# Performance work log

Measured on AMD Instinct MI355X. Metric: run time of the kernel, lower is better.

The kernel has to match this reference:

```python
import jax, jax.numpy as jnp
import numpy as np

B, S, H = 8, 512, 1024          # batch, seq_len, hidden_size
T, K, FF = 8, 2, 4096           # num_thoughts, top_k, ffn dim (4*H)
NH = 8                          # combiner attention heads
HD = H // NH
CREATIVITY = 1.0


def setup_inputs() -> dict:
    key = jax.random.key(0)
    ks = jax.random.split(key, 16)
    s = 0.02
    return {
        "hidden_states": jax.random.normal(ks[0], (B, S, H), jnp.float32),
        # router
        "router_w": jax.random.normal(ks[1], (H, T), jnp.float32) * s,
        "router_b": jnp.zeros((T,), jnp.float32),
        # thought branch FFNs (one per thought)
        "W1": jax.random.normal(ks[2], (T, H, FF), jnp.float32) * s,
        "b1": jnp.zeros((T, FF), jnp.float32),
        "W2": jax.random.normal(ks[3], (T, FF, H), jnp.float32) * s,
        "b2": jnp.zeros((T, H), jnp.float32),
        # attention combiner (MultiheadAttention proj weights)
        "Wq": jax.random.normal(ks[4], (H, H), jnp.float32) * s,
        "bq": jnp.zeros((H,), jnp.float32),
        "Wk": jax.random.normal(ks[5], (H, H), jnp.float32) * s,
        "bk": jnp.zeros((H,), jnp.float32),
        "Wv": jax.random.normal(ks[6], (H, H), jnp.float32) * s,
        "bv": jnp.zeros((H,), jnp.float32),
        "Wo": jax.random.normal(ks[7], (H, H), jnp.float32) * s,
        "bo": jnp.zeros((H,), jnp.float32),
    }


def reference(hidden_states, router_w, router_b, W1, b1, W2, b2,
              Wq, bq, Wk, bk, Wv, bv, Wo, bo):
    # ---- router: mean-pool -> linear -> softmax -> top-k ----
    pooled = hidden_states.mean(axis=1)                       # [B,H]
    router_probs = jax.nn.softmax(pooled @ router_w + router_b, axis=-1)  # [B,T]
    top_p, top_i = jax.lax.top_k(router_probs, K)             # [B,K]
    weights = jax.nn.softmax(top_p, axis=-1)                  # renormalized active weights [B,K]

    # ---- grouped branch FFN (gather expert weights, batched GEMMs) ----
    h = jnp.einsum('bsh,bkhf->bksf', hidden_states, W1[top_i]) + b1[top_i][:, :, None, :]
    h = jax.nn.gelu(h, approximate=False)
    branch_out = jnp.einsum('bksf,bkfh->bksh', h, W2[top_i]) + b2[top_i][:, :, None, :]
    branch_out = branch_out * CREATIVITY                      # [B,K,S,H]

    # ---- attention combiner over flattened thoughts [B, K*S, H] ----
    L = K * S
    flat = branch_out.reshape(B, L, H)
    q = (flat @ Wq + bq).reshape(B, L, NH, HD)
    k = (flat @ Wk + bk).reshape(B, L, NH, HD)
    v = (flat @ Wv + bv).reshape(B, L, NH, HD)
    scores = jnp.einsum('blhd,bmhd->bhlm', q, k) / jnp.sqrt(jnp.float32(HD))
    attn = jax.nn.softmax(scores, axis=-1)
    ctx = jnp.einsum('bhlm,bmhd->blhd', attn, v).reshape(B, L, H)
    attended = (ctx @ Wo + bo).reshape(B, K, S, H)

    combined = jnp.einsum('bksh,bk->bsh', attended, weights)  # [B,S,H]

    # ---- metrics ----
    entropy = jnp.mean(-jnp.sum(router_probs * jnp.log(router_probs + 1e-8), axis=1))
    a = branch_out[:, 0].reshape(B, -1)
    b_ = branch_out[:, 1].reshape(B, -1)
    cos = jnp.sum(a * b_, -1) / jnp.maximum(
        jnp.linalg.norm(a, axis=-1) * jnp.linalg.norm(b_, axis=-1), 1e-8)
    diversity = jnp.mean(1.0 - cos)
    return combined, entropy, diversity
```

## Files before the change

kernel.cpp:

```cpp
#include <hip/hip_runtime.h>
#include <hip/hip_bf16.h>
#include <math.h>

typedef float f32x4 __attribute__((ext_vector_type(4)));
typedef short s16x8 __attribute__((ext_vector_type(8)));
typedef short s16x4 __attribute__((ext_vector_type(4)));
typedef unsigned int u32;

#define DEVI __device__ __forceinline__

#define Bn   8
#define Sn   512
#define Hn   1024
#define Tn   8
#define Kn   2
#define FFn  4096
#define NHn  8
#define HDn  128
#define Ln   1024
#define OUT_COMBINED 4194304

DEVI unsigned short f2bf(float x) {
  __hip_bfloat16 h = __float2bfloat16(x);
  union { __hip_bfloat16 h; unsigned short u; } cv; cv.h = h; return cv.u;
}
DEVI float bf2f(unsigned short u) {
  union { u32 i; float f; } cv; cv.i = ((u32)u) << 16; return cv.f;
}
DEVI float gelu_f(float x) {
  float t = x * x * x;
  float y = 0.7978845608028654f * x + 0.03567740813f * t;
  float e = exp2f(2.8853900817779268f * y);
  return x - x / (e + 1.0f);
}

typedef __attribute__((address_space(3))) u32 lds_u32;
typedef __attribute__((address_space(1))) u32 glb_u32;
DEVI void gload16(const void* g, void* l) {
  __builtin_amdgcn_global_load_lds((const glb_u32*)g, (lds_u32*)l, 16, 0, 0);
}

__global__ __launch_bounds__(256) void pool_part_k(const float* __restrict__ hid, float* __restrict__ part)
{
  const int b = blockIdx.x, scn = blockIdx.y;
  const int hh = threadIdx.x * 4;
  float4 acc = make_float4(0.f, 0.f, 0.f, 0.f);
  const float* base = hid + ((long)b * Sn + (long)scn * 128) * Hn + hh;
  for (int s = 0; s < 128; ++s) {
    float4 v = *(const float4*)(base + (long)s * Hn);
    acc.x += v.x; acc.y += v.y; acc.z += v.z; acc.w += v.w;
  }
  *(float4*)(part + ((long)(scn * Bn + b)) * Hn + hh) = acc;
}

__global__ __launch_bounds__(256) void pool_final_k(const float* __restrict__ part, float* __restrict__ pooled)
{
  const int i = blockIdx.x * 256 + threadIdx.x;
  float s = 0.f;
  for (int sc = 0; sc < 4; ++sc) s += part[sc * (Bn * Hn) + i];
  pooled[i] = s * (1.f / (float)Sn);
}

__global__ __launch_bounds__(256) void router_k(
    const float* __restrict__ pooled, const float* __restrict__ rw, const float* __restrict__ rb,
    float* __restrict__ probs, int* __restrict__ topi, float* __restrict__ wts,
    int* __restrict__ flags, float* __restrict__ entropy_out)
{
  __shared__ float partial[256];
  __shared__ float lg[64];
  __shared__ int sfl[8];
  __shared__ float sent[8];
  const int tid = threadIdx.x;
  const int bt = tid & 63, slice = tid >> 6;
  const int b = bt >> 3, t = bt & 7;
  if (tid < 8) sfl[tid] = 0;
  float acc = 0.f;
  const float* pb = pooled + b * Hn;
  for (int i = slice * 256; i < slice * 256 + 256; ++i) acc += pb[i] * rw[i * Tn + t];
  partial[tid] = acc;
  __syncthreads();
  if (tid < 64) lg[tid] = rb[t] + partial[tid] + partial[tid + 64] + partial[tid + 128] + partial[tid + 192];
  __syncthreads();
  if (tid < 64 && t == 0) {
    float p[8];
    float mx = lg[b * 8];
    for (int i = 1; i < 8; ++i) mx = fmaxf(mx, lg[b * 8 + i]);
    float ssum = 0.f;
    for (int i = 0; i < 8; ++i) { p[i] = expf(lg[b * 8 + i] - mx); ssum += p[i]; }
    float ent = 0.f;
    for (int i = 0; i < 8; ++i) { p[i] /= ssum; ent -= p[i] * logf(p[i] + 1e-8f); probs[b * 8 + i] = p[i]; }
    sent[b] = ent;
    int i1 = 0;
    for (int i = 1; i < 8; ++i) if (p[i] > p[i1]) i1 = i;
    int i2 = (i1 == 0) ? 1 : 0;
    for (int i = 0; i < 8; ++i) if (i != i1 && p[i] > p[i2]) i2 = i;
    float w0 = 1.f / (1.f + expf(p[i2] - p[i1]));
    float w1 = 1.f / (1.f + expf(p[i1] - p[i2]));
    topi[b * 2] = i1; topi[b * 2 + 1] = i2;
    wts[b * 2] = w0; wts[b * 2 + 1] = w1;
    atomicOr(&sfl[i1], 1); atomicOr(&sfl[i2], 1);
  }
  __syncthreads();
  if (tid < 8) flags[tid] = sfl[tid];
  if (tid == 0) {
    float e = 0.f;
    for (int i = 0; i < 8; ++i) e += sent[i];
    entropy_out[0] = e * (1.f / (float)Bn);
  }
}

__global__ __launch_bounds__(256) void cvt_k(const float* __restrict__ in, unsigned short* __restrict__ out)
{
  const long i = ((long)blockIdx.x * 256 + threadIdx.x) * 4;
  float4 v = *(const float4*)(in + i);
  s16x4 o;
  o[0] = (short)f2bf(v.x); o[1] = (short)f2bf(v.y); o[2] = (short)f2bf(v.z); o[3] = (short)f2bf(v.w);
  *(s16x4*)(out + i) = o;
}

__global__ __launch_bounds__(256) void bias3_k(const float* __restrict__ bq, const float* __restrict__ bk,
                                               const float* __restrict__ bv, float* __restrict__ o)
{
  const int i = blockIdx.x * 256 + threadIdx.x;
  o[i] = bq[i]; o[i + 1024] = bk[i]; o[i + 2048] = bv[i];
}

__global__ __launch_bounds__(256) void transpose_k(const float* __restrict__ Win, unsigned short* __restrict__ Wout,
                                                   int Kd, int N, long sIn, long sOut, const int* __restrict__ flags)
{
  const int t = blockIdx.z;
  if (flags && flags[t] == 0) return;
  __shared__ float tile[64][65];
  const float* in = Win + (long)t * sIn;
  unsigned short* out = Wout + (long)t * sOut;
  const int kb = blockIdx.y * 64, nb = blockIdx.x * 64;
  const int tx = threadIdx.x & 15, ty = threadIdx.x >> 4;
  #pragma unroll
  for (int i = 0; i < 4; ++i) {
    const int r = ty + i * 16;
    float4 v = *(const float4*)(in + (long)(kb + r) * N + nb + tx * 4);
    tile[r][tx * 4 + 0] = v.x; tile[r][tx * 4 + 1] = v.y;
    tile[r][tx * 4 + 2] = v.z; tile[r][tx * 4 + 3] = v.w;
  }
  __syncthreads();
  #pragma unroll
  for (int i = 0; i < 4; ++i) {
    const int n = ty + i * 16;
    s16x4 o;
    #pragma unroll
    for (int j = 0; j < 4; ++j) o[j] = (short)f2bf(tile[tx * 4 + j][n]);
    *(s16x4*)(out + (long)(nb + n) * Kd + kb + tx * 4) = o;
  }
}

template<int EPI, int OUTMODE>
__global__ __launch_bounds__(256, 2) void gemmT_k(
    const unsigned short* __restrict__ A0, const unsigned short* __restrict__ Bt0,
    const float* __restrict__ bias0, unsigned short* __restrict__ C0,
    int N, int Kd,
    const int* __restrict__ topi, int kTop,
    long sA_b, long sA_p, long sBt_t, int sBias_t, long sC_p)
{
  __shared__ __align__(16) char smem[73728];
  char* const Ab = smem;
  char* const Bb = smem + 49152;

  const int gx = gridDim.x, gy = gridDim.y;
  const int nwg = gx * gy * gridDim.z;
  const int hw = blockIdx.x + gx * (blockIdx.y + gy * blockIdx.z);
  const int q = nwg >> 3, r = nwg & 7;
  const int xcd = hw & 7, sub = hw >> 3;
  int lin = (xcd < r ? xcd * (q + 1) : r * (q + 1) + (xcd - r) * q) + sub;
  const int bx = lin % gx; lin /= gx;
  const int by = lin % gy;
  const int bz = lin / gy;

  const int bidx = kTop ? (bz / kTop) : 0;
  const int te = topi ? topi[bz] : 0;
  const unsigned short* A = A0 + (long)bidx * sA_b + (long)bz * sA_p;
  const unsigned short* Bt = Bt0 + (long)te * sBt_t;
  const float* bias = bias0 + (long)te * sBias_t;
  unsigned short* C = C0 + (long)bz * sC_p;

  const int m0 = by * 256;
  const int n0 = bx * 128;
  const int tid = threadIdx.x;
  const int lane = tid & 63, w = tid >> 6;
  const int wm = w >> 1, wn = w & 1;
  const int rA = lane & 15, g = lane >> 4;

  const int sr = lane >> 2;
  const int sc = lane & 3;
  const int csw = (sc ^ ((sr & 3) ^ ((sr >> 2) & 3))) * 8;
  const unsigned short* gAw = A + (long)(m0 + w * 64 + sr) * Kd + csw;
  const unsigned short* gBw = Bt + (long)(n0 + w * 32 + sr) * Kd + csw;
  const int ldso = lane << 4;

  const int sl = (rA & 3) ^ ((rA >> 2) & 3);
  int aoff[8], boff[4];
  #pragma unroll
  for (int mi = 0; mi < 8; ++mi)
    aoff[mi] = (wm * 128 + mi * 16 + rA) * 64 + ((g ^ sl) << 4);
  #pragma unroll
  for (int nj = 0; nj < 4; ++nj)
    boff[nj] = (wn * 64 + nj * 16 + rA) * 64 + ((g ^ sl) << 4);

  f32x4 acc[8][4];
  const f32x4 zero = {0.f, 0.f, 0.f, 0.f};
  #pragma unroll
  for (int i = 0; i < 8; ++i)
    #pragma unroll
    for (int j = 0; j < 4; ++j) acc[i][j] = zero;

  const int nt = Kd >> 5;

  auto stageA = [&](int kt2, int buf, int i) {
    gload16(gAw + (long)i * 16 * Kd + kt2 * 32, Ab + buf * 16384 + w * 4096 + i * 1024 + ldso);
  };
  auto stageB = [&](int kt2, int buf, int i) {
    gload16(gBw + (long)i * 16 * Kd + kt2 * 32, Bb + buf * 8192 + w * 2048 + i * 1024 + ldso);
  };

  #pragma unroll
  for (int j = 0; j < 2; ++j) {
    stageA(j, j, 0); stageA(j, j, 1); stageB(j, j, 0);
    stageA(j, j, 2); stageA(j, j, 3); stageB(j, j, 1);
  }
  asm volatile("s_waitcnt vmcnt(6)" ::: "memory");
  __builtin_amdgcn_s_barrier();

  int cb = 0, fb = 2;
  for (int kt = 0; kt < nt; ++kt) {
    const char* pa = Ab + cb * 16384;
    const char* pb = Bb + cb * 8192;
    const bool st = (kt + 2 < nt);
    const int ft = kt + 2;

    s16x8 af[8], bf[4];
    #pragma unroll
    for (int mi = 0; mi < 4; ++mi) af[mi] = *(const s16x8*)(pa + aoff[mi]);
    #pragma unroll
    for (int nj = 0; nj < 4; ++nj) bf[nj] = *(const s16x8*)(pb + boff[nj]);
    if (st) { stageA(ft, fb, 0); stageA(ft, fb, 1); stageB(ft, fb, 0); }
    #pragma unroll
    for (int mi = 0; mi < 4; ++mi) af[4 + mi] = *(const s16x8*)(pa + aoff[4 + mi]);
    if (st) { stageA(ft, fb, 2); stageA(ft, fb, 3); stageB(ft, fb, 1); }

    __builtin_amdgcn_s_setprio(1);
    #pragma unroll
    for (int mi = 0; mi < 8; ++mi)
      #pragma unroll
      for (int nj = 0; nj < 4; ++nj)
        acc[mi][nj] = __builtin_amdgcn_mfma_f32_16x16x32_bf16(af[mi], bf[nj], acc[mi][nj], 0, 0, 0);
    __builtin_amdgcn_s_setprio(0);

    if (st)                asm volatile("s_waitcnt vmcnt(6) lgkmcnt(0)" ::: "memory");
    else if (kt + 1 < nt)  asm volatile("s_waitcnt vmcnt(0) lgkmcnt(0)" ::: "memory");
    else                   asm volatile("s_waitcnt lgkmcnt(0)" ::: "memory");
    __builtin_amdgcn_s_barrier();
    cb = (cb + 1 == 3) ? 0 : cb + 1;
    fb = (fb + 1 == 3) ? 0 : fb + 1;
  }

  __syncthreads();

  unsigned short* et = (unsigned short*)(smem + w * 9216);
  const int r4 = (lane >> 4) << 2;
  const int nbase = n0 + wn * 64;
  const int seg = (OUTMODE == 1) ? (nbase >> 10) : 0;
  const int erow = lane >> 3, echunk = lane & 7;
  float bv[4];
  #pragma unroll
  for (int nj = 0; nj < 4; ++nj) bv[nj] = bias[nbase + nj * 16 + rA];

  #pragma unroll
  for (int p = 0; p < 2; ++p) {
    #pragma unroll
    for (int nj = 0; nj < 4; ++nj) {
      #pragma unroll
      for (int mi2 = 0; mi2 < 4; ++mi2) {
        #pragma unroll
        for (int j = 0; j < 4; ++j) {
          float x = acc[p * 4 + mi2][nj][j] + bv[nj];
          if (EPI == 1) x = gelu_f(x);
          const int mrl = mi2 * 16 + r4 + j;
          const int ncl = nj * 16 + rA;
          if (OUTMODE == 0 || seg < 2) et[mrl * 72 + ncl] = f2bf(x);
          else                         et[ncl * 72 + mrl] = f2bf(x);
        }
      }
    }
    const long mrow0 = m0 + wm * 128 + p * 64;
    if (OUTMODE == 0) {
      #pragma unroll
      for (int rr = 0; rr < 8; ++rr) {
        const int row = rr * 8 + erow;
        s16x8 v = *(const s16x8*)(et + row * 72 + echunk * 8);
        *(s16x8*)(C + (mrow0 + row) * N + nbase + echunk * 8) = v;
      }
    } else {
      const int nseg = nbase & 1023;
      if (seg < 2) {
        unsigned short* dst = C + (long)seg * 8388608;
        #pragma unroll
        for (int rr = 0; rr < 8; ++rr) {
          const int row = rr * 8 + erow;
          s16x8 v = *(const s16x8*)(et + row * 72 + echunk * 8);
          *(s16x8*)(dst + (mrow0 + row) * 1024 + nseg + echunk * 8) = v;
        }
      } else {
        unsigned short* vtp = C + 16777216;
        const int bb = (int)(mrow0 >> 10);
        const int ltok0 = (int)(mrow0 & 1023);
        #pragma unroll
        for (int rr = 0; rr < 8; ++rr) {
          const int nrow = rr * 8 + erow;
          s16x8 v = *(const s16x8*)(et + nrow * 72 + echunk * 8);
          *(s16x8*)(vtp + ((long)(bb * 1024 + nseg + nrow)) * 1024 + ltok0 + echunk * 8) = v;
        }
      }
    }
  }
}

__global__ __launch_bounds__(256) void flash_k(
    const unsigned short* __restrict__ q, const unsigned short* __restrict__ k,
    const unsigned short* __restrict__ vt, unsigned short* __restrict__ ctx)
{
  __shared__ unsigned short Ks[64 * 128];
  __shared__ unsigned short Vs[128 * 64];
  __shared__ unsigned short Ps[4][32 * 72];
  const int qt = blockIdx.x, h = blockIdx.y, b = blockIdx.z;
  const int tid = threadIdx.x, lane = tid & 63, w = tid >> 6;
  const int rA = lane & 15, g = lane >> 4;
  const int q0w = qt * 128 + w * 32;

  s16x8 qf[2][4];
  #pragma unroll
  for (int qi = 0; qi < 2; ++qi) {
    const unsigned short* qp = q + ((long)(b * Ln + q0w + qi * 16 + rA)) * Hn + h * HDn + g * 8;
    #pragma unroll
    for (int kk = 0; kk < 4; ++kk) qf[qi][kk] = *(const s16x8*)(qp + kk * 32);
  }

  f32x4 o[2][8];
  const f32x4 zero = {0.f, 0.f, 0.f, 0.f};
  #pragma unroll
  for (int qi = 0; qi < 2; ++qi)
    #pragma unroll
    for (int nn = 0; nn < 8; ++nn) o[qi][nn] = zero;
  float lrun[2][4];
  #pragma unroll
  for (int qi = 0; qi < 2; ++qi)
    #pragma unroll
    for (int j = 0; j < 4; ++j) lrun[qi][j] = 0.f;
  float m = 0.f;

  const float sc2 = 0.08838834764831845f * 1.4426950408889634f;

  const int krow0 = w * 16 + g;
  const int kc = lane & 15;
  const int vrow0 = w * 32 + (lane >> 3);
  const int vc = lane & 7;

  for (int kvt = 0; kvt < 16; ++kvt) {
    const int kv0 = kvt * 64;
    __syncthreads();
    #pragma unroll
    for (int qq = 0; qq < 4; ++qq) {
      const int rk = krow0 + qq * 4;
      gload16(k + ((long)(b * Ln + kv0 + rk)) * Hn + h * HDn + ((kc ^ (rk & 7)) * 8),
              (char*)Ks + w * 4096 + qq * 1024);
      const int rv = vrow0 + qq * 8;
      gload16(vt + ((long)(b * 1024 + h * HDn + rv)) * Ln + kv0 + ((vc ^ (rv & 7)) * 8),
              (char*)Vs + w * 4096 + qq * 1024);
    }
    __syncthreads();

    f32x4 sacc[2][4];
    #pragma unroll
    for (int qi = 0; qi < 2; ++qi)
      #pragma unroll
      for (int nj = 0; nj < 4; ++nj) sacc[qi][nj] = zero;
    #pragma unroll
    for (int kk = 0; kk < 4; ++kk) {
      #pragma unroll
      for (int nj = 0; nj < 4; ++nj) {
        const int row = nj * 16 + rA;
        const int byt = row * 256 + (((kk * 4 + g) ^ (row & 7)) << 4);
        s16x8 kf = *(const s16x8*)((const char*)Ks + byt);
        sacc[0][nj] = __builtin_amdgcn_mfma_f32_16x16x32_bf16(qf[0][kk], kf, sacc[0][nj], 0, 0, 0);
        sacc[1][nj] = __builtin_amdgcn_mfma_f32_16x16x32_bf16(qf[1][kk], kf, sacc[1][nj], 0, 0, 0);
      }
    }

    float vmax = -3.0e38f;
    #pragma unroll
    for (int qi = 0; qi < 2; ++qi)
      #pragma unroll
      for (int nj = 0; nj < 4; ++nj)
        #pragma unroll
        for (int j = 0; j < 4; ++j) {
          const float s = sacc[qi][nj][j] * sc2;
          sacc[qi][nj][j] = s;
          vmax = fmaxf(vmax, s);
        }
    if (!__all(vmax <= m + 8.0f)) {
      float mn = vmax;
      #pragma unroll
      for (int mm = 1; mm < 64; mm <<= 1) mn = fmaxf(mn, __shfl_xor(mn, mm, 64));
      const float al = exp2f(m - mn);
      #pragma unroll
      for (int qi = 0; qi < 2; ++qi) {
        #pragma unroll
        for (int nn = 0; nn < 8; ++nn)
          #pragma unroll
          for (int j = 0; j < 4; ++j) o[qi][nn][j] *= al;
        #pragma unroll
        for (int j = 0; j < 4; ++j) lrun[qi][j] *= al;
      }
      m = mn;
    }
    #pragma unroll
    for (int qi = 0; qi < 2; ++qi)
      #pragma unroll
      for (int j = 0; j < 4; ++j) {
        float p0 = exp2f(sacc[qi][0][j] - m);
        float p1 = exp2f(sacc[qi][1][j] - m);
        float p2 = exp2f(sacc[qi][2][j] - m);
        float p3 = exp2f(sacc[qi][3][j] - m);
        lrun[qi][j] += (p0 + p1) + (p2 + p3);
        const int prow = (qi * 16 + g * 4 + j) * 72;
        Ps[w][prow + 0 * 16 + rA] = f2bf(p0);
        Ps[w][prow + 1 * 16 + rA] = f2bf(p1);
        Ps[w][prow + 2 * 16 + rA] = f2bf(p2);
        Ps[w][prow + 3 * 16 + rA] = f2bf(p3);
      }

    s16x8 pf[2][2];
    #pragma unroll
    for (int qi = 0; qi < 2; ++qi)
      #pragma unroll
      for (int kk2 = 0; kk2 < 2; ++kk2)
        pf[qi][kk2] = *(const s16x8*)(&Ps[w][(qi * 16 + rA) * 72 + kk2 * 32 + g * 8]);
    #pragma unroll
    for (int kk2 = 0; kk2 < 2; ++kk2) {
      #pragma unroll
      for (int nn = 0; nn < 8; ++nn) {
        const int row = nn * 16 + rA;
        const int byt = row * 128 + (((kk2 * 4 + g) ^ (row & 7)) << 4);
        s16x8 vf = *(const s16x8*)((const char*)Vs + byt);
        o[0][nn] = __builtin_amdgcn_mfma_f32_16x16x32_bf16(pf[0][kk2], vf, o[0][nn], 0, 0, 0);
        o[1][nn] = __builtin_amdgcn_mfma_f32_16x16x32_bf16(pf[1][kk2], vf, o[1][nn], 0, 0, 0);
      }
    }
  }

  float linv[2][4];
  #pragma unroll
  for (int qi = 0; qi < 2; ++qi)
    #pragma unroll
    for (int j = 0; j < 4; ++j) {
      float l = lrun[qi][j];
      #pragma unroll
      for (int mm = 1; mm < 16; mm <<= 1) l += __shfl_xor(l, mm, 64);
      linv[qi][j] = 1.0f / l;
    }
  #pragma unroll
  for (int qi = 0; qi < 2; ++qi)
    #pragma unroll
    for (int nn = 0; nn < 8; ++nn)
      #pragma unroll
      for (int j = 0; j < 4; ++j) {
        const int row = q0w + qi * 16 + g * 4 + j;
        ctx[((long)(b * Ln + row)) * Hn + h * HDn + nn * 16 + rA] = f2bf(o[qi][nn][j] * linv[qi][j]);
      }
}

__global__ __launch_bounds__(256) void div_part_k(const unsigned short* __restrict__ br, float* __restrict__ part)
{
  const int b = blockIdx.y, ch = blockIdx.x;
  const unsigned short* a = br + (long)b * (2L * Sn * Hn);
  const unsigned short* c = a + (long)Sn * Hn;
  const int base = ch * 16384 + threadIdx.x * 8;
  float dot = 0.f, na = 0.f, nb = 0.f;
  #pragma unroll
  for (int i = 0; i < 8; ++i) {
    const int idx = base + i * 2048;
    s16x8 av = *(const s16x8*)(a + idx);
    s16x8 cv = *(const s16x8*)(c + idx);
    #pragma unroll
    for (int e = 0; e < 8; ++e) {
      float fa = bf2f((unsigned short)av[e]);
      float fc = bf2f((unsigned short)cv[e]);
      dot += fa * fc; na += fa * fa; nb += fc * fc;
    }
  }
  #pragma unroll
  for (int mm = 1; mm < 64; mm <<= 1) {
    dot += __shfl_xor(dot, mm, 64);
    na  += __shfl_xor(na, mm, 64);
    nb  += __shfl_xor(nb, mm, 64);
  }
  __shared__ float red[12];
  const int lane = threadIdx.x & 63, w = threadIdx.x >> 6;
  if (lane == 0) { red[w * 3] = dot; red[w * 3 + 1] = na; red[w * 3 + 2] = nb; }
  __syncthreads();
  if (threadIdx.x == 0) {
    float d = 0, x = 0, y = 0;
    for (int i = 0; i < 4; ++i) { d += red[i * 3]; x += red[i * 3 + 1]; y += red[i * 3 + 2]; }
    float* op = part + ((long)(b * 32 + ch)) * 3;
    op[0] = d; op[1] = x; op[2] = y;
  }
}

__global__ __launch_bounds__(64) void div_final_k(const float* __restrict__ part, float* __restrict__ outp)
{
  __shared__ float cosr[8];
  const int tid = threadIdx.x;
  if (tid < 8) {
    float d = 0, x = 0, y = 0;
    for (int i = 0; i < 32; ++i) {
      const float* p = part + ((long)(tid * 32 + i)) * 3;
      d += p[0]; x += p[1]; y += p[2];
    }
    cosr[tid] = d / fmaxf(sqrtf(x) * sqrtf(y), 1e-8f);
  }
  __syncthreads();
  if (tid == 0) {
    float s = 0.f;
    for (int i = 0; i < 8; ++i) s += 1.f - cosr[i];
    outp[0] = s * (1.f / 8.f);
  }
}

__global__ __launch_bounds__(256) void combine_k(const unsigned short* __restrict__ att,
                                                 const float* __restrict__ wts, float* __restrict__ out)
{
  const long i = ((long)blockIdx.x * 256 + threadIdx.x) * 8;
  const int b = (int)(i >> 19);
  const long rem = i & 524287;
  const unsigned short* a0 = att + (long)b * (2L * Sn * Hn) + rem;
  const unsigned short* a1 = a0 + (long)Sn * Hn;
  const float w0 = wts[b * 2], w1 = wts[b * 2 + 1];
  s16x8 v0 = *(const s16x8*)a0;
  s16x8 v1 = *(const s16x8*)a1;
  float r[8];
  #pragma unroll
  for (int e = 0; e < 8; ++e) r[e] = w0 * bf2f((unsigned short)v0[e]) + w1 * bf2f((unsigned short)v1[e]);
  *(float4*)(out + i)     = make_float4(r[0], r[1], r[2], r[3]);
  *(float4*)(out + i + 4) = make_float4(r[4], r[5], r[6], r[7]);
}

extern "C" void kernel_launch(void* const* d_in, const int* in_sizes, int n_in,
                              void* d_out, int out_size, void* d_ws, size_t ws_size,
                              hipStream_t stream)
{
  (void)in_sizes; (void)n_in; (void)out_size; (void)ws_size;
  const float* hidden   = (const float*)d_in[0];
  const float* router_w = (const float*)d_in[1];
  const float* router_b = (const float*)d_in[2];
  const float* W1 = (const float*)d_in[3];
  const float* b1 = (const float*)d_in[4];
  const float* W2 = (const float*)d_in[5];
  const float* b2 = (const float*)d_in[6];
  const float* Wq = (const float*)d_in[7];
  const float* bq = (const float*)d_in[8];
  const float* Wk = (const float*)d_in[9];
  const float* bk = (const float*)d_in[10];
  const float* Wv = (const float*)d_in[11];
  const float* bv = (const float*)d_in[12];
  const float* Wo = (const float*)d_in[13];
  const float* bo = (const float*)d_in[14];
  float* out = (float*)d_out;

  char* ws = (char*)d_ws;
  float* pooled  = (float*)(ws);
  float* ppart   = (float*)(ws + 32768);
  float* probs   = (float*)(ws + 163840);
  int*   topi    = (int*)  (ws + 164096);
  float* wts     = (float*)(ws + 164352);
  int*   flags   = (int*)  (ws + 164608);
  float* dpart   = (float*)(ws + 164864);
  float* qkvbias = (float*)(ws + 167936);
  unsigned short* hid_bf = (unsigned short*)(ws + 262144);
  unsigned short* Wt     = (unsigned short*)(ws + 262144 + 8388608);
  unsigned short* hbuf   = (unsigned short*)(ws + 262144 + 8388608 + 67108864);
  unsigned short* br     = (unsigned short*)(ws + 262144 + 8388608 + 134217728);
  unsigned short* wqkvo  = (unsigned short*)(ws + 262144 + 8388608 + 134217728 + 16777216);
  unsigned short* qb  = Wt;
  unsigned short* kbf = Wt + 8388608;
  unsigned short* vt  = Wt + 16777216;
  unsigned short* ctx = hbuf;
  unsigned short* att = hbuf + 8388608;
  unsigned short* wqt = wqkvo;
  unsigned short* wkt = wqkvo + 1048576;
  unsigned short* wvt = wqkvo + 2097152;
  unsigned short* wot = wqkvo + 3145728;

  pool_part_k<<<dim3(Bn, 4), 256, 0, stream>>>(hidden, ppart);
  pool_final_k<<<dim3(32), 256, 0, stream>>>(ppart, pooled);
  router_k<<<1, 256, 0, stream>>>(pooled, router_w, router_b, probs, topi, wts, flags, out + OUT_COMBINED);

  cvt_k<<<4096, 256, 0, stream>>>(hidden, hid_bf);
  bias3_k<<<4, 256, 0, stream>>>(bq, bk, bv, qkvbias);
  transpose_k<<<dim3(64, 16, Tn), 256, 0, stream>>>(W1, Wt, Hn, FFn, (long)Hn * FFn, (long)FFn * Hn, flags);
  transpose_k<<<dim3(16, 16, 1), 256, 0, stream>>>(Wq, wqt, Hn, Hn, 0, 0, nullptr);
  transpose_k<<<dim3(16, 16, 1), 256, 0, stream>>>(Wk, wkt, Hn, Hn, 0, 0, nullptr);
  transpose_k<<<dim3(16, 16, 1), 256, 0, stream>>>(Wv, wvt, Hn, Hn, 0, 0, nullptr);
  transpose_k<<<dim3(16, 16, 1), 256, 0, stream>>>(Wo, wot, Hn, Hn, 0, 0, nullptr);

  gemmT_k<1, 0><<<dim3(FFn / 128, Sn / 256, 16), 256, 0, stream>>>(
      hid_bf, Wt, b1, hbuf, FFn, Hn, topi, 2,
      (long)Sn * Hn, 0L, (long)FFn * Hn, FFn, (long)Sn * FFn);

  transpose_k<<<dim3(16, 64, Tn), 256, 0, stream>>>(W2, Wt, FFn, Hn, (long)FFn * Hn, (long)Hn * FFn, flags);

  gemmT_k<0, 0><<<dim3(Hn / 128, Sn / 256, 16), 256, 0, stream>>>(
      hbuf, Wt, b2, br, Hn, FFn, topi, 2,
      0L, (long)Sn * FFn, (long)Hn * FFn, Hn, (long)Sn * Hn);

  div_part_k<<<dim3(32, Bn), 256, 0, stream>>>(br, dpart);
  div_final_k<<<1, 64, 0, stream>>>(dpart, out + OUT_COMBINED + 1);

  gemmT_k<0, 1><<<dim3(3072 / 128, (Bn * Ln) / 256, 1), 256, 0, stream>>>(
      br, wqkvo, qkvbias, qb, 3072, Hn, nullptr, 0, 0L, 0L, 0L, 0, 0L);

  flash_k<<<dim3(Ln / 128, NHn, Bn), 256, 0, stream>>>(qb, kbf, vt, ctx);

  gemmT_k<0, 0><<<dim3(Hn / 128, (Bn * Ln) / 256, 1), 256, 0, stream>>>(
      ctx, wot, bo, att, Hn, Hn, nullptr, 0, 0L, 0L, 0L, 0, 0L);

  combine_k<<<2048, 256, 0, stream>>>(att, wts, out);
}
```

Baseline: 517.7 us.

## Use 256x256 8-wave GEMM tiles with split-K for FFN2

```diff
diff --git a/kernel.cpp b/kernel.cpp
--- a/kernel.cpp
+++ b/kernel.cpp
@@ -123,6 +123,7 @@
 {
   const int i = blockIdx.x * 256 + threadIdx.x;
   o[i] = bq[i]; o[i + 1024] = bk[i]; o[i + 2048] = bv[i];
+  o[i + 3072] = 0.f;
 }
 
 __global__ __launch_bounds__(256) void transpose_k(const float* __restrict__ Win, unsigned short* __restrict__ Wout,
@@ -153,17 +154,18 @@
   }
 }
 
-template<int EPI, int OUTMODE>
-__global__ __launch_bounds__(256, 2) void gemmT_k(
+template<int EPI, int OUTMODE, int KSPLIT>
+__global__ __launch_bounds__(512, 1) void gemm8_k(
     const unsigned short* __restrict__ A0, const unsigned short* __restrict__ Bt0,
-    const float* __restrict__ bias0, unsigned short* __restrict__ C0,
-    int N, int Kd,
+    const float* __restrict__ bias0, const float* __restrict__ zbias,
+    unsigned short* __restrict__ C0,
+    int N, int Kd, int Klen,
     const int* __restrict__ topi, int kTop,
-    long sA_b, long sA_p, long sBt_t, int sBias_t, long sC_p)
-{
-  __shared__ __align__(16) char smem[73728];
+    long sA_b, long sA_p, long sBt_t, int sBias_t, long sC_p, long sC_k)
+{
+  __shared__ __align__(16) char smem[131072];
   char* const Ab = smem;
-  char* const Bb = smem + 49152;
+  char* const Bb = smem + 65536;
 
   const int gx = gridDim.x, gy = gridDim.y;
   const int nwg = gx * gy * gridDim.z;
@@ -175,35 +177,51 @@
   const int by = lin % gy;
   const int bz = lin / gy;
 
-  const int bidx = kTop ? (bz / kTop) : 0;
-  const int te = topi ? topi[bz] : 0;
-  const unsigned short* A = A0 + (long)bidx * sA_b + (long)bz * sA_p;
-  const unsigned short* Bt = Bt0 + (long)te * sBt_t;
-  const float* bias = bias0 + (long)te * sBias_t;
-  unsigned short* C = C0 + (long)bz * sC_p;
+  const int zp = KSPLIT ? (bz >> 1) : bz;
+  const int ks = KSPLIT ? (bz & 1) : 0;
+  const int bidx = kTop ? (zp / kTop) : 0;
+  const int te = topi ? topi[zp] : 0;
+  const unsigned short* A = A0 + (long)bidx * sA_b + (long)zp * sA_p + ks * 2048;
+  const unsigned short* Bt = Bt0 + (long)te * sBt_t + ks * 2048;
+  const float* bias = (KSPLIT && ks) ? zbias : (bias0 + (long)te * sBias_t);
+  unsigned short* C = C0 + (long)zp * sC_p + (long)ks * sC_k;
 
   const int m0 = by * 256;
-  const int n0 = bx * 128;
+  const int n0 = bx * 256;
   const int tid = threadIdx.x;
   const int lane = tid & 63, w = tid >> 6;
-  const int wm = w >> 1, wn = w & 1;
+  const int wm = w >> 2, wn = w & 3;
   const int rA = lane & 15, g = lane >> 4;
 
-  const int sr = lane >> 2;
-  const int sc = lane & 3;
-  const int csw = (sc ^ ((sr & 3) ^ ((sr >> 2) & 3))) * 8;
-  const unsigned short* gAw = A + (long)(m0 + w * 64 + sr) * Kd + csw;
-  const unsigned short* gBw = Bt + (long)(n0 + w * 32 + sr) * Kd + csw;
-  const int ldso = lane << 4;
-
-  const int sl = (rA & 3) ^ ((rA >> 2) & 3);
+  const int srow = tid >> 2;
+  const int sc = tid & 3;
+  const int csw = (sc ^ ((srow & 3) ^ ((srow >> 2) & 3))) * 8;
+  const unsigned short* gA0p = A + (long)(m0 + srow) * Kd + csw;
+  const unsigned short* gA1p = A + (long)(m0 + srow + 128) * Kd + csw;
+  const unsigned short* gB0p = Bt + (long)(n0 + srow) * Kd + csw;
+  const unsigned short* gB1p = Bt + (long)(n0 + srow + 128) * Kd + csw;
+
+  auto stA = [&](int kt2, int buf, int kh) {
+    const long ko = (long)kt2 * 64 + kh * 32;
+    char* d = Ab + buf * 32768 + kh * 16384 + tid * 16;
+    gload16(gA0p + ko, d);
+    gload16(gA1p + ko, d + 8192);
+  };
+  auto stB = [&](int kt2, int buf, int kh) {
+    const long ko = (long)kt2 * 64 + kh * 32;
+    char* d = Bb + buf * 32768 + kh * 16384 + tid * 16;
+    gload16(gB0p + ko, d);
+    gload16(gB1p + ko, d + 8192);
+  };
+
+  const int chsw = (g ^ ((rA & 3) ^ ((rA >> 2) & 3))) << 4;
   int aoff[8], boff[4];
   #pragma unroll
   for (int mi = 0; mi < 8; ++mi)
-    aoff[mi] = (wm * 128 + mi * 16 + rA) * 64 + ((g ^ sl) << 4);
+    aoff[mi] = (wm * 128 + mi * 16 + rA) * 64 + chsw;
   #pragma unroll
   for (int nj = 0; nj < 4; ++nj)
-    boff[nj] = (wn * 64 + nj * 16 + rA) * 64 + ((g ^ sl) << 4);
+    boff[nj] = (wn * 64 + nj * 16 + rA) * 64 + chsw;
 
   f32x4 acc[8][4];
   const f32x4 zero = {0.f, 0.f, 0.f, 0.f};
@@ -212,60 +230,99 @@
     #pragma unroll
     for (int j = 0; j < 4; ++j) acc[i][j] = zero;
 
-  const int nt = Kd >> 5;
-
-  auto stageA = [&](int kt2, int buf, int i) {
-    gload16(gAw + (long)i * 16 * Kd + kt2 * 32, Ab + buf * 16384 + w * 4096 + i * 1024 + ldso);
-  };
-  auto stageB = [&](int kt2, int buf, int i) {
-    gload16(gBw + (long)i * 16 * Kd + kt2 * 32, Bb + buf * 8192 + w * 2048 + i * 1024 + ldso);
-  };
-
-  #pragma unroll
-  for (int j = 0; j < 2; ++j) {
-    stageA(j, j, 0); stageA(j, j, 1); stageB(j, j, 0);
-    stageA(j, j, 2); stageA(j, j, 3); stageB(j, j, 1);
-  }
-  asm volatile("s_waitcnt vmcnt(6)" ::: "memory");
+  const int nt = Klen >> 6;
+
+  stA(0, 0, 0); stB(0, 0, 0); stA(0, 0, 1); stB(0, 0, 1);
+  asm volatile("s_waitcnt vmcnt(4)" ::: "memory");
   __builtin_amdgcn_s_barrier();
 
-  int cb = 0, fb = 2;
   for (int kt = 0; kt < nt; ++kt) {
-    const char* pa = Ab + cb * 16384;
-    const char* pb = Bb + cb * 8192;
-    const bool st = (kt + 2 < nt);
-    const int ft = kt + 2;
-
-    s16x8 af[8], bf[4];
-    #pragma unroll
-    for (int mi = 0; mi < 4; ++mi) af[mi] = *(const s16x8*)(pa + aoff[mi]);
-    #pragma unroll
-    for (int nj = 0; nj < 4; ++nj) bf[nj] = *(const s16x8*)(pb + boff[nj]);
-    if (st) { stageA(ft, fb, 0); stageA(ft, fb, 1); stageB(ft, fb, 0); }
-    #pragma unroll
-    for (int mi = 0; mi < 4; ++mi) af[4 + mi] = *(const s16x8*)(pa + aoff[4 + mi]);
-    if (st) { stageA(ft, fb, 2); stageA(ft, fb, 3); stageB(ft, fb, 1); }
-
+    const char* paA = Ab + (kt & 1) * 32768;
+    const char* paB = Bb + (kt & 1) * 32768;
+    const int fb = (kt & 1) ^ 1;
+    const bool st = (kt + 1 < nt);
+    s16x8 af[4], bf[4];
+
+    #pragma unroll
+    for (int mi = 0; mi < 4; ++mi) af[mi] = *(const s16x8*)(paA + aoff[mi]);
+    #pragma unroll
+    for (int nj = 0; nj < 4; ++nj) bf[nj] = *(const s16x8*)(paB + boff[nj]);
+    if (st) stA(kt + 1, fb, 0);
+    __builtin_amdgcn_sched_barrier(0);
+    __builtin_amdgcn_s_barrier();
+    asm volatile("s_waitcnt lgkmcnt(0)" ::: "memory");
+    __builtin_amdgcn_sched_barrier(0);
     __builtin_amdgcn_s_setprio(1);
     #pragma unroll
-    for (int mi = 0; mi < 8; ++mi)
+    for (int mi = 0; mi < 4; ++mi)
       #pragma unroll
       for (int nj = 0; nj < 4; ++nj)
         acc[mi][nj] = __builtin_amdgcn_mfma_f32_16x16x32_bf16(af[mi], bf[nj], acc[mi][nj], 0, 0, 0);
     __builtin_amdgcn_s_setprio(0);
-
-    if (st)                asm volatile("s_waitcnt vmcnt(6) lgkmcnt(0)" ::: "memory");
-    else if (kt + 1 < nt)  asm volatile("s_waitcnt vmcnt(0) lgkmcnt(0)" ::: "memory");
-    else                   asm volatile("s_waitcnt lgkmcnt(0)" ::: "memory");
+    __builtin_amdgcn_sched_barrier(0);
     __builtin_amdgcn_s_barrier();
-    cb = (cb + 1 == 3) ? 0 : cb + 1;
-    fb = (fb + 1 == 3) ? 0 : fb + 1;
+
+    #pragma unroll
+    for (int mi = 0; mi < 4; ++mi) af[mi] = *(const s16x8*)(paA + aoff[4 + mi]);
+    if (st) stB(kt + 1, fb, 0);
+    __builtin_amdgcn_sched_barrier(0);
+    __builtin_amdgcn_s_barrier();
+    asm volatile("s_waitcnt lgkmcnt(0)" ::: "memory");
+    __builtin_amdgcn_sched_barrier(0);
+    __builtin_amdgcn_s_setprio(1);
+    #pragma unroll
+    for (int mi = 0; mi < 4; ++mi)
+      #pragma unroll
+      for (int nj = 0; nj < 4; ++nj)
+        acc[4 + mi][nj] = __builtin_amdgcn_mfma_f32_16x16x32_bf16(af[mi], bf[nj], acc[4 + mi][nj], 0, 0, 0);
+    __builtin_amdgcn_s_setprio(0);
+    __builtin_amdgcn_sched_barrier(0);
+    if (st) asm volatile("s_waitcnt vmcnt(4)" ::: "memory");
+    else    asm volatile("s_waitcnt vmcnt(0)" ::: "memory");
+    __builtin_amdgcn_s_barrier();
+
+    #pragma unroll
+    for (int mi = 0; mi < 4; ++mi) af[mi] = *(const s16x8*)(paA + 16384 + aoff[mi]);
+    #pragma unroll
+    for (int nj = 0; nj < 4; ++nj) bf[nj] = *(const s16x8*)(paB + 16384 + boff[nj]);
+    if (st) stA(kt + 1, fb, 1);
+    __builtin_amdgcn_sched_barrier(0);
+    __builtin_amdgcn_s_barrier();
+    asm volatile("s_waitcnt lgkmcnt(0)" ::: "memory");
+    __builtin_amdgcn_sched_barrier(0);
+    __builtin_amdgcn_s_setprio(1);
+    #pragma unroll
+    for (int mi = 0; mi < 4; ++mi)
+      #pragma unroll
+      for (int nj = 0; nj < 4; ++nj)
+        acc[mi][nj] = __builtin_amdgcn_mfma_f32_16x16x32_bf16(af[mi], bf[nj], acc[mi][nj], 0, 0, 0);
+    __builtin_amdgcn_s_setprio(0);
+    __builtin_amdgcn_sched_barrier(0);
+    __builtin_amdgcn_s_barrier();
+
+    #pragma unroll
+    for (int mi = 0; mi < 4; ++mi) af[mi] = *(const s16x8*)(paA + 16384 + aoff[4 + mi]);
+    if (st) stB(kt + 1, fb, 1);
+    __builtin_amdgcn_sched_barrier(0);
+    __builtin_amdgcn_s_barrier();
+    asm volatile("s_waitcnt lgkmcnt(0)" ::: "memory");
+    __builtin_amdgcn_sched_barrier(0);
+    __builtin_amdgcn_s_setprio(1);
+    #pragma unroll
+    for (int mi = 0; mi < 4; ++mi)
+      #pragma unroll
+      for (int nj = 0; nj < 4; ++nj)
+        acc[4 + mi][nj] = __builtin_amdgcn_mfma_f32_16x16x32_bf16(af[mi], bf[nj], acc[4 + mi][nj], 0, 0, 0);
+    __builtin_amdgcn_s_setprio(0);
+    __builtin_amdgcn_sched_barrier(0);
+    if (st) asm volatile("s_waitcnt vmcnt(4)" ::: "memory");
+    __builtin_amdgcn_s_barrier();
   }
 
   __syncthreads();
 
   unsigned short* et = (unsigned short*)(smem + w * 9216);
-  const int r4 = (lane >> 4) << 2;
+  const int r4 = g << 2;
   const int nbase = n0 + wn * 64;
   const int seg = (OUTMODE == 1) ? (nbase >> 10) : 0;
   const int erow = lane >> 3, echunk = lane & 7;
@@ -323,6 +380,162 @@
   }
 }
 
+__global__ __launch_bounds__(256) void ffn2red_k(const unsigned short* __restrict__ fpart,
+                                                 unsigned short* __restrict__ br)
+{
+  const long i = ((long)blockIdx.x * 256 + threadIdx.x) * 8;
+  s16x8 a = *(const s16x8*)(fpart + i);
+  s16x8 b = *(const s16x8*)(fpart + 8388608 + i);
+  s16x8 o;
+  #pragma unroll
+  for (int e = 0; e < 8; ++e)
+    o[e] = (short)f2bf(bf2f((unsigned short)a[e]) + bf2f((unsigned short)b[e]));
+  *(s16x8*)(br + i) = o;
+}
+
+template<int EPI, int OUTMODE>
+__global__ __launch_bounds__(256, 2) void gemmT_k(
+    const unsigned short* __restrict__ A0, const unsigned short* __restrict__ Bt0,
+    const float* __restrict__ bias0, unsigned short* __restrict__ C0,
+    int N, int Kd,
+    const int* __restrict__ topi, int kTop,
+    long sA_b, long sA_p, long sBt_t, int sBias_t, long sC_p)
+{
+  __shared__ __align__(16) char smem[73728];
+  char* const Ab = smem;
+  char* const Bb = smem + 49152;
+
+  const int gx = gridDim.x, gy = gridDim.y;
+  const int nwg = gx * gy * gridDim.z;
+  const int hw = blockIdx.x + gx * (blockIdx.y + gy * blockIdx.z);
+  const int q = nwg >> 3, r = nwg & 7;
+  const int xcd = hw & 7, sub = hw >> 3;
+  int lin = (xcd < r ? xcd * (q + 1) : r * (q + 1) + (xcd - r) * q) + sub;
+  const int bx = lin % gx; lin /= gx;
+  const int by = lin % gy;
+  const int bz = lin / gy;
+
+  const int bidx = kTop ? (bz / kTop) : 0;
+  const int te = topi ? topi[bz] : 0;
+  const unsigned short* A = A0 + (long)bidx * sA_b + (long)bz * sA_p;
+  const unsigned short* Bt = Bt0 + (long)te * sBt_t;
+  const float* bias = bias0 + (long)te * sBias_t;
+  unsigned short* C = C0 + (long)bz * sC_p;
+
+  const int m0 = by * 256;
+  const int n0 = bx * 128;
+  const int tid = threadIdx.x;
+  const int lane = tid & 63, w = tid >> 6;
+  const int wm = w >> 1, wn = w & 1;
+  const int rA = lane & 15, g = lane >> 4;
+
+  const int sr = lane >> 2;
+  const int sc = lane & 3;
+  const int csw = (sc ^ ((sr & 3) ^ ((sr >> 2) & 3))) * 8;
+  const unsigned short* gAw = A + (long)(m0 + w * 64 + sr) * Kd + csw;
+  const unsigned short* gBw = Bt + (long)(n0 + w * 32 + sr) * Kd + csw;
+  const int ldso = lane << 4;
+
+  const int sl = (rA & 3) ^ ((rA >> 2) & 3);
+  int aoff[8], boff[4];
+  #pragma unroll
+  for (int mi = 0; mi < 8; ++mi)
+    aoff[mi] = (wm * 128 + mi * 16 + rA) * 64 + ((g ^ sl) << 4);
+  #pragma unroll
+  for (int nj = 0; nj < 4; ++nj)
+    boff[nj] = (wn * 64 + nj * 16 + rA) * 64 + ((g ^ sl) << 4);
+
+  f32x4 acc[8][4];
+  const f32x4 zero = {0.f, 0.f, 0.f, 0.f};
+  #pragma unroll
+  for (int i = 0; i < 8; ++i)
+    #pragma unroll
+    for (int j = 0; j < 4; ++j) acc[i][j] = zero;
+
+  const int nt = Kd >> 5;
+
+  auto stageA = [&](int kt2, int buf, int i) {
+    gload16(gAw + (long)i * 16 * Kd + kt2 * 32, Ab + buf * 16384 + w * 4096 + i * 1024 + ldso);
+  };
+  auto stageB = [&](int kt2, int buf, int i) {
+    gload16(gBw + (long)i * 16 * Kd + kt2 * 32, Bb + buf * 8192 + w * 2048 + i * 1024 + ldso);
+  };
+
+  #pragma unroll
+  for (int j = 0; j < 2; ++j) {
+    stageA(j, j, 0); stageA(j, j, 1); stageB(j, j, 0);
+    stageA(j, j, 2); stageA(j, j, 3); stageB(j, j, 1);
+  }
+  asm volatile("s_waitcnt vmcnt(6)" ::: "memory");
+  __builtin_amdgcn_s_barrier();
+
+  int cb = 0, fb = 2;
+  for (int kt = 0; kt < nt; ++kt) {
+    const char* pa = Ab + cb * 16384;
+    const char* pb = Bb + cb * 8192;
+    const bool st = (kt + 2 < nt);
+    const int ft = kt + 2;
+
+    s16x8 af[8], bf[4];
+    #pragma unroll
+    for (int mi = 0; mi < 4; ++mi) af[mi] = *(const s16x8*)(pa + aoff[mi]);
+    #pragma unroll
+    for (int nj = 0; nj < 4; ++nj) bf[nj] = *(const s16x8*)(pb + boff[nj]);
+    if (st) { stageA(ft, fb, 0); stageA(ft, fb, 1); stageB(ft, fb, 0); }
+    #pragma unroll
+    for (int mi = 0; mi < 4; ++mi) af[4 + mi] = *(const s16x8*)(pa + aoff[4 + mi]);
+    if (st) { stageA(ft, fb, 2); stageA(ft, fb, 3); stageB(ft, fb, 1); }
+
+    __builtin_amdgcn_s_setprio(1);
+    #pragma unroll
+    for (int mi = 0; mi < 8; ++mi)
+      #pragma unroll
+      for (int nj = 0; nj < 4; ++nj)
+        acc[mi][nj] = __builtin_amdgcn_mfma_f32_16x16x32_bf16(af[mi], bf[nj], acc[mi][nj], 0, 0, 0);
+    __builtin_amdgcn_s_setprio(0);
+
+    if (st)                asm volatile("s_waitcnt vmcnt(6) lgkmcnt(0)" ::: "memory");
+    else if (kt + 1 < nt)  asm volatile("s_waitcnt vmcnt(0) lgkmcnt(0)" ::: "memory");
+    else                   asm volatile("s_waitcnt lgkmcnt(0)" ::: "memory");
+    __builtin_amdgcn_s_barrier();
+    cb = (cb + 1 == 3) ? 0 : cb + 1;
+    fb = (fb + 1 == 3) ? 0 : fb + 1;
+  }
+
+  __syncthreads();
+
+  unsigned short* et = (unsigned short*)(smem + w * 9216);
+  const int r4 = g << 2;
+  const int nbase = n0 + wn * 64;
+  const int erow = lane >> 3, echunk = lane & 7;
+  float bv[4];
+  #pragma unroll
+  for (int nj = 0; nj < 4; ++nj) bv[nj] = bias[nbase + nj * 16 + rA];
+
+  #pragma unroll
+  for (int p = 0; p < 2; ++p) {
+    #pragma unroll
+    for (int nj = 0; nj < 4; ++nj) {
+      #pragma unroll
+      for (int mi2 = 0; mi2 < 4; ++mi2) {
+        #pragma unroll
+        for (int j = 0; j < 4; ++j) {
+          float x = acc[p * 4 + mi2][nj][j] + bv[nj];
+          if (EPI == 1) x = gelu_f(x);
+          et[(mi2 * 16 + r4 + j) * 72 + nj * 16 + rA] = f2bf(x);
+        }
+      }
+    }
+    const long mrow0 = m0 + wm * 128 + p * 64;
+    #pragma unroll
+    for (int rr = 0; rr < 8; ++rr) {
+      const int row = rr * 8 + erow;
+      s16x8 v = *(const s16x8*)(et + row * 72 + echunk * 8);
+      *(s16x8*)(C + (mrow0 + row) * N + nbase + echunk * 8) = v;
+    }
+  }
+}
+
 __global__ __launch_bounds__(256) void flash_k(
     const unsigned short* __restrict__ q, const unsigned short* __restrict__ k,
     const unsigned short* __restrict__ vt, unsigned short* __restrict__ ctx)
@@ -583,11 +796,13 @@
   int*   flags   = (int*)  (ws + 164608);
   float* dpart   = (float*)(ws + 164864);
   float* qkvbias = (float*)(ws + 167936);
+  float* zbias   = qkvbias + 3072;
   unsigned short* hid_bf = (unsigned short*)(ws + 262144);
   unsigned short* Wt     = (unsigned short*)(ws + 262144 + 8388608);
   unsigned short* hbuf   = (unsigned short*)(ws + 262144 + 8388608 + 67108864);
   unsigned short* br     = (unsigned short*)(ws + 262144 + 8388608 + 134217728);
   unsigned short* wqkvo  = (unsigned short*)(ws + 262144 + 8388608 + 134217728 + 16777216);
+  unsigned short* fpart  = (unsigned short*)(ws + 262144 + 8388608 + 134217728 + 16777216 + 8388608);
   unsigned short* qb  = Wt;
   unsigned short* kbf = Wt + 8388608;
   unsigned short* vt  = Wt + 16777216;
@@ -610,21 +825,23 @@
   transpose_k<<<dim3(16, 16, 1), 256, 0, stream>>>(Wv, wvt, Hn, Hn, 0, 0, nullptr);
   transpose_k<<<dim3(16, 16, 1), 256, 0, stream>>>(Wo, wot, Hn, Hn, 0, 0, nullptr);
 
-  gemmT_k<1, 0><<<dim3(FFn / 128, Sn / 256, 16), 256, 0, stream>>>(
-      hid_bf, Wt, b1, hbuf, FFn, Hn, topi, 2,
-      (long)Sn * Hn, 0L, (long)FFn * Hn, FFn, (long)Sn * FFn);
+  gemm8_k<1, 0, 0><<<dim3(FFn / 256, Sn / 256, 16), 512, 0, stream>>>(
+      hid_bf, Wt, b1, zbias, hbuf, FFn, Hn, Hn, topi, 2,
+      (long)Sn * Hn, 0L, (long)FFn * Hn, FFn, (long)Sn * FFn, 0L);
 
   transpose_k<<<dim3(16, 64, Tn), 256, 0, stream>>>(W2, Wt, FFn, Hn, (long)FFn * Hn, (long)Hn * FFn, flags);
 
-  gemmT_k<0, 0><<<dim3(Hn / 128, Sn / 256, 16), 256, 0, stream>>>(
-      hbuf, Wt, b2, br, Hn, FFn, topi, 2,
-      0L, (long)Sn * FFn, (long)Hn * FFn, Hn, (long)Sn * Hn);
+  gemm8_k<0, 0, 1><<<dim3(Hn / 256, Sn / 256, 32), 512, 0, stream>>>(
+      hbuf, Wt, b2, zbias, fpart, Hn, FFn, FFn / 2, topi, 2,
+      0L, (long)Sn * FFn, (long)Hn * FFn, Hn, (long)Sn * Hn, 8388608L);
+  ffn2red_k<<<4096, 256, 0, stream>>>(fpart, br);
 
   div_part_k<<<dim3(32, Bn), 256, 0, stream>>>(br, dpart);
   div_final_k<<<1, 64, 0, stream>>>(dpart, out + OUT_COMBINED + 1);
 
-  gemmT_k<0, 1><<<dim3(3072 / 128, (Bn * Ln) / 256, 1), 256, 0, stream>>>(
-      br, wqkvo, qkvbias, qb, 3072, Hn, nullptr, 0, 0L, 0L, 0L, 0, 0L);
+  gemm8_k<0, 1, 0><<<dim3(3072 / 256, (Bn * Ln) / 256, 1), 512, 0, stream>>>(
+      br, wqkvo, qkvbias, zbias, qb, 3072, Hn, Hn, nullptr, 0,
+      0L, 0L, 0L, 0, 0L, 0L);
 
   flash_k<<<dim3(Ln / 128, NHn, Bn), 256, 0, stream>>>(qb, kbf, vt, ctx);
 
```

Result: no change. 523.2 us (+1.1%).

## Double-buffer K tiles in flash attention and overlap loads with compute

Applied to the files above, without the earlier changes.

```diff
diff --git a/kernel.cpp b/kernel.cpp
--- a/kernel.cpp
+++ b/kernel.cpp
@@ -191,12 +191,12 @@
 
   const int sr = lane >> 2;
   const int sc = lane & 3;
-  const int csw = (sc ^ ((sr & 3) ^ ((sr >> 2) & 3))) * 8;
+  const int csw = (sc ^ ((sr >> 1) & 3)) * 8;
   const unsigned short* gAw = A + (long)(m0 + w * 64 + sr) * Kd + csw;
   const unsigned short* gBw = Bt + (long)(n0 + w * 32 + sr) * Kd + csw;
   const int ldso = lane << 4;
 
-  const int sl = (rA & 3) ^ ((rA >> 2) & 3);
+  const int sl = (rA >> 1) & 3;
   int aoff[8], boff[4];
   #pragma unroll
   for (int mi = 0; mi < 8; ++mi)
@@ -265,7 +265,7 @@
   __syncthreads();
 
   unsigned short* et = (unsigned short*)(smem + w * 9216);
-  const int r4 = (lane >> 4) << 2;
+  const int r4 = g << 2;
   const int nbase = n0 + wn * 64;
   const int seg = (OUTMODE == 1) ? (nbase >> 10) : 0;
   const int erow = lane >> 3, echunk = lane & 7;
@@ -327,10 +327,13 @@
     const unsigned short* __restrict__ q, const unsigned short* __restrict__ k,
     const unsigned short* __restrict__ vt, unsigned short* __restrict__ ctx)
 {
-  __shared__ unsigned short Ks[64 * 128];
+  __shared__ unsigned short K2[2][64 * 128];
   __shared__ unsigned short Vs[128 * 64];
   __shared__ unsigned short Ps[4][32 * 72];
-  const int qt = blockIdx.x, h = blockIdx.y, b = blockIdx.z;
+  const int L = blockIdx.x;
+  const int qt = L >> 6;
+  const int hb = (((L >> 3) & 7) << 3) + (L & 7);
+  const int h = hb & 7, b = hb >> 3;
   const int tid = threadIdx.x, lane = tid & 63, w = tid >> 6;
   const int rA = lane & 15, g = lane >> 4;
   const int q0w = qt * 128 + w * 32;
@@ -342,6 +345,7 @@
     #pragma unroll
     for (int kk = 0; kk < 4; ++kk) qf[qi][kk] = *(const s16x8*)(qp + kk * 32);
   }
+  asm volatile("s_waitcnt vmcnt(0)" ::: "memory");
 
   f32x4 o[2][8];
   const f32x4 zero = {0.f, 0.f, 0.f, 0.f};
@@ -363,36 +367,53 @@
   const int vrow0 = w * 32 + (lane >> 3);
   const int vc = lane & 7;
 
-  for (int kvt = 0; kvt < 16; ++kvt) {
-    const int kv0 = kvt * 64;
-    __syncthreads();
+  auto issueK = [&](int kvt2, int buf) {
+    const int kv0 = kvt2 * 64;
     #pragma unroll
     for (int qq = 0; qq < 4; ++qq) {
       const int rk = krow0 + qq * 4;
       gload16(k + ((long)(b * Ln + kv0 + rk)) * Hn + h * HDn + ((kc ^ (rk & 7)) * 8),
-              (char*)Ks + w * 4096 + qq * 1024);
+              (char*)K2[buf] + w * 4096 + qq * 1024);
+    }
+  };
+  auto issueV = [&](int kvt2) {
+    const int kv0 = kvt2 * 64;
+    #pragma unroll
+    for (int qq = 0; qq < 4; ++qq) {
       const int rv = vrow0 + qq * 8;
       gload16(vt + ((long)(b * 1024 + h * HDn + rv)) * Ln + kv0 + ((vc ^ (rv & 7)) * 8),
               (char*)Vs + w * 4096 + qq * 1024);
     }
-    __syncthreads();
+  };
+
+  issueK(0, 0);
+  asm volatile("s_waitcnt vmcnt(0)" ::: "memory");
+  __builtin_amdgcn_s_barrier();
+
+  for (int kvt = 0; kvt < 16; ++kvt) {
+    const bool st = (kvt + 1 < 16);
+    const char* Kcur = (const char*)K2[kvt & 1];
+    issueV(kvt);
+    if (st) issueK(kvt + 1, (kvt + 1) & 1);
 
     f32x4 sacc[2][4];
     #pragma unroll
     for (int qi = 0; qi < 2; ++qi)
       #pragma unroll
       for (int nj = 0; nj < 4; ++nj) sacc[qi][nj] = zero;
+    __builtin_amdgcn_s_setprio(1);
     #pragma unroll
     for (int kk = 0; kk < 4; ++kk) {
       #pragma unroll
       for (int nj = 0; nj < 4; ++nj) {
         const int row = nj * 16 + rA;
         const int byt = row * 256 + (((kk * 4 + g) ^ (row & 7)) << 4);
-        s16x8 kf = *(const s16x8*)((const char*)Ks + byt);
+        s16x8 kf = *(const s16x8*)(Kcur + byt);
         sacc[0][nj] = __builtin_amdgcn_mfma_f32_16x16x32_bf16(qf[0][kk], kf, sacc[0][nj], 0, 0, 0);
         sacc[1][nj] = __builtin_amdgcn_mfma_f32_16x16x32_bf16(qf[1][kk], kf, sacc[1][nj], 0, 0, 0);
       }
     }
+    __builtin_amdgcn_s_setprio(0);
 
     float vmax = -3.0e38f;
     #pragma unroll
@@ -421,6 +442,11 @@
       }
       m = mn;
     }
+
+    if (st) asm volatile("s_waitcnt vmcnt(4)" ::: "memory");
+    else    asm volatile("s_waitcnt vmcnt(0)" ::: "memory");
+    __builtin_amdgcn_s_barrier();
+
     #pragma unroll
     for (int qi = 0; qi < 2; ++qi)
       #pragma unroll
@@ -443,6 +469,7 @@
       #pragma unroll
       for (int kk2 = 0; kk2 < 2; ++kk2)
         pf[qi][kk2] = *(const s16x8*)(&Ps[w][(qi * 16 + rA) * 72 + kk2 * 32 + g * 8]);
+    __builtin_amdgcn_s_setprio(1);
     #pragma unroll
     for (int kk2 = 0; kk2 < 2; ++kk2) {
       #pragma unroll
@@ -454,6 +481,11 @@
         o[1][nn] = __builtin_amdgcn_mfma_f32_16x16x32_bf16(pf[1][kk2], vf, o[1][nn], 0, 0, 0);
       }
     }
+    __builtin_amdgcn_s_setprio(0);
+
+    if (st) asm volatile("s_waitcnt vmcnt(0) lgkmcnt(0)" ::: "memory");
+    else    asm volatile("s_waitcnt lgkmcnt(0)" ::: "memory");
+    __builtin_amdgcn_s_barrier();
   }
 
   float linv[2][4];
@@ -626,7 +658,7 @@
   gemmT_k<0, 1><<<dim3(3072 / 128, (Bn * Ln) / 256, 1), 256, 0, stream>>>(
       br, wqkvo, qkvbias, qb, 3072, Hn, nullptr, 0, 0L, 0L, 0L, 0, 0L);
 
-  flash_k<<<dim3(Ln / 128, NHn, Bn), 256, 0, stream>>>(qb, kbf, vt, ctx);
+  flash_k<<<dim3(512), 256, 0, stream>>>(qb, kbf, vt, ctx);
 
   gemmT_k<0, 0><<<dim3(Hn / 128, (Bn * Ln) / 256, 1), 256, 0, stream>>>(
       ctx, wot, bo, att, Hn, Hn, nullptr, 0, 0L, 0L, 0L, 0, 0L);
```

Result: no change. 517.1 us, median of 2 (-0.1%).
